# Kernel optimization log

Hardware: AMD Instinct MI355X
Metric: run time of the kernel (lower is better)

Reference implementation:

```python
import jax, jax.numpy as jnp
import numpy as np

NUM_HEADS = 8  # from init_kwargs

def _conv1x1(x, W, b):
    # x: [B, Cin, H, W], W: [Cout, Cin], b: [Cout]  (nn.Conv2d kernel_size=1)
    return jnp.einsum('bchw,oc->bohw', x, W) + b[None, :, None, None]

def setup_inputs() -> dict:
    key = jax.random.key(0)
    ks = jax.random.split(key, 9)
    B, C, H, W = 8, 256, 32, 32
    Ck, Cv, Co = 256, 256, 256
    s = 1.0 / np.sqrt(C)
    return {
        'x':  jax.random.normal(ks[0], (B, C, H, W), dtype=jnp.float32),
        'Wq': jax.random.normal(ks[1], (Ck, C), dtype=jnp.float32) * s,
        'bq': jax.random.normal(ks[2], (Ck,), dtype=jnp.float32) * 0.02,
        'Wk': jax.random.normal(ks[3], (Ck, C), dtype=jnp.float32) * s,
        'bk': jax.random.normal(ks[4], (Ck,), dtype=jnp.float32) * 0.02,
        'Wv': jax.random.normal(ks[5], (Cv, C), dtype=jnp.float32) * s,
        'bv': jax.random.normal(ks[6], (Cv,), dtype=jnp.float32) * 0.02,
        'Wo': jax.random.normal(ks[7], (Co, Cv), dtype=jnp.float32) * s,
        'bo': jax.random.normal(ks[8], (Co,), dtype=jnp.float32) * 0.02,
    }

def reference(x, Wq, bq, Wk, bk, Wv, bv, Wo, bo):
    B, C, H, W = x.shape
    q = _conv1x1(x, Wq, bq)  # [B, Ck, H, W]
    k = _conv1x1(x, Wk, bk)  # [B, Ck, H, W]
    v = _conv1x1(x, Wv, bv)  # [B, Cv, H, W]
    nh = NUM_HEADS
    dk = q.shape[1] // nh
    dv = v.shape[1] // nh
    N = H * W
    # split heads, flatten spatial dims into sequence
    q = q.reshape(B, nh, dk, N) * (dk ** -0.5)
    k = k.reshape(B, nh, dk, N)
    v = v.reshape(B, nh, dv, N)
    logits = jnp.einsum('bhdn,bhdm->bhnm', q, k)        # [B, nh, N, N]
    attn = jax.nn.softmax(logits, axis=-1)
    o = jnp.einsum('bhnm,bhdm->bhdn', attn, v)           # [B, nh, dv, N]
    o = o.reshape(B, nh * dv, H, W)
    return _conv1x1(o, Wo, bo)                           # [B, Co, H, W]
```

## Files before the change

### kernel.cpp

```cpp
#include <hip/hip_runtime.h>
#include <math.h>

typedef unsigned short u16;
typedef __attribute__((ext_vector_type(8))) unsigned short u16x8;
typedef __attribute__((ext_vector_type(8))) short s16x8;
typedef __attribute__((ext_vector_type(4))) float f32x4;

#define QK_SCALE (0.17677669529663687f * 1.4426950408889634f)

__device__ __forceinline__ unsigned cvt2(float lo, float hi) {
  unsigned r;
  asm("v_cvt_pk_bf16_f32 %0, %1, %2" : "=v"(r) : "v"(lo), "v"(hi));
  return r;
}
__device__ __forceinline__ u16 f2bf(float f) { return (u16)cvt2(f, f); }
__device__ __forceinline__ u16x8 ld16(const void* p) { u16x8 v; __builtin_memcpy(&v, p, 16); return v; }
__device__ __forceinline__ void st16(void* p, u16x8 v) { __builtin_memcpy(p, &v, 16); }
__device__ __forceinline__ void st16s(void* p, s16x8 v) { __builtin_memcpy(p, &v, 16); }
__device__ __forceinline__ void st4(void* p, unsigned v) { __builtin_memcpy(p, &v, 4); }
__device__ __forceinline__ f32x4 ldf4(const void* p) { f32x4 v; __builtin_memcpy(&v, p, 16); return v; }
__device__ __forceinline__ void stf4(void* p, f32x4 v) { __builtin_memcpy(p, &v, 16); }
__device__ __forceinline__ s16x8 frag16(const void* p) { s16x8 v; __builtin_memcpy(&v, p, 16); return v; }
__device__ __forceinline__ s16x8 pack8(f32x4 lo, f32x4 hi) {
  union { unsigned u[4]; s16x8 s; } c;
  c.u[0] = cvt2(lo.x, lo.y); c.u[1] = cvt2(lo.z, lo.w);
  c.u[2] = cvt2(hi.x, hi.y); c.u[3] = cvt2(hi.z, hi.w);
  return c.s;
}

__global__ __launch_bounds__(256) void r18_qkv(
    const float* __restrict__ x,
    const float* __restrict__ Wq, const float* __restrict__ bq,
    const float* __restrict__ Wk, const float* __restrict__ bk,
    const float* __restrict__ Wv, const float* __restrict__ bv,
    u16* __restrict__ qo, u16* __restrict__ ko, u16* __restrict__ vo)
{
  __shared__ u16 xt[64][264];
  __shared__ u16 wlds[192][40];

  const int t = threadIdx.x;
  const int ntile = blockIdx.x, hp = blockIdx.y, b = blockIdx.z;
  const int n0 = ntile * 64, h0 = hp * 2;
  const int w = t >> 6, lane = t & 63, l15 = lane & 15, quad = lane >> 4;

  {
    const float* xrow = x + ((size_t)b * 256 + t) * 1024 + n0;
#pragma unroll
    for (int i = 0; i < 64; i += 4) {
      const f32x4 a = ldf4(xrow + i);
      xt[i + 0][t] = f2bf(a.x); xt[i + 1][t] = f2bf(a.y);
      xt[i + 2][t] = f2bf(a.z); xt[i + 3][t] = f2bf(a.w);
    }
  }

  f32x4 acc[12];
#pragma unroll
  for (int i = 0; i < 12; ++i) acc[i] = (f32x4){0.f, 0.f, 0.f, 0.f};

  for (int ks = 0; ks < 8; ++ks) {
    __syncthreads();
    if (t < 192) {
      const int m = t >> 6, hh = (t >> 5) & 1, r = t & 31;
      const float* M = (m == 0) ? Wq : (m == 1) ? Wk : Wv;
      const float* src = M + (size_t)((h0 + hh) * 32 + r) * 256 + ks * 32;
      st16s(&wlds[t][0],  pack8(ldf4(src),      ldf4(src + 4)));
      st16s(&wlds[t][8],  pack8(ldf4(src + 8),  ldf4(src + 12)));
      st16s(&wlds[t][16], pack8(ldf4(src + 16), ldf4(src + 20)));
      st16s(&wlds[t][24], pack8(ldf4(src + 24), ldf4(src + 28)));
    }
    __syncthreads();

    const s16x8 bfrag = frag16(&xt[w * 16 + l15][ks * 32 + quad * 8]);
#pragma unroll
    for (int mt = 0; mt < 12; ++mt) {
      const s16x8 af = frag16(&wlds[mt * 16 + l15][quad * 8]);
      acc[mt] = __builtin_amdgcn_mfma_f32_16x16x32_bf16(af, bfrag, acc[mt], 0, 0, 0);
    }
  }

  const int n = n0 + w * 16 + l15;
  const int sig = n & 127;
  const int nperm = (n & ~127) | ((sig & 15) << 3) | (sig >> 4);
#pragma unroll
  for (int hh = 0; hh < 2; ++hh) {
    const int h = h0 + hh;
    const size_t bh = (size_t)(b * 8 + h);
    u16* qrow = qo + (bh * 1024 + n) * 32;
    u16* krow = ko + (bh * 1024 + n) * 32;
#pragma unroll
    for (int half = 0; half < 2; ++half) {
      const int d0 = half * 16 + quad * 4;
      const f32x4 aq = acc[hh * 2 + half];
      const f32x4 ak = acc[4 + hh * 2 + half];
      const f32x4 av = acc[8 + hh * 2 + half];
      st4(qrow + d0,     cvt2((aq.x + bq[h * 32 + d0 + 0]) * QK_SCALE,
                              (aq.y + bq[h * 32 + d0 + 1]) * QK_SCALE));
      st4(qrow + d0 + 2, cvt2((aq.z + bq[h * 32 + d0 + 2]) * QK_SCALE,
                              (aq.w + bq[h * 32 + d0 + 3]) * QK_SCALE));
      st4(krow + d0,     cvt2(ak.x + bk[h * 32 + d0 + 0],
                              ak.y + bk[h * 32 + d0 + 1]));
      st4(krow + d0 + 2, cvt2(ak.z + bk[h * 32 + d0 + 2],
                              ak.w + bk[h * 32 + d0 + 3]));
#pragma unroll
      for (int rr = 0; rr < 4; ++rr) {
        const int d = d0 + rr;
        vo[(bh * 32 + d) * 1024 + nperm] = f2bf(av[rr] + bv[h * 32 + d]);
      }
    }
  }
}

__global__ __launch_bounds__(256) void r18_attn(
    const u16* __restrict__ qw, const u16* __restrict__ kw,
    const u16* __restrict__ vw, float* __restrict__ out)
{
  __shared__ __align__(16) char smem[36352];
  u16 (*klds)[40]  = (u16(*)[40])smem;
  u16 (*vlds)[136] = (u16(*)[136])(smem + 10240);
  u16 (*plds)[136] = (u16(*)[136])(smem + 18944);
  float (*otf)[72] = (float(*)[72])smem;

  const int t = threadIdx.x;
  const int qtile = blockIdx.x;
  const int bh = blockIdx.y;
  const int w = t >> 6, lane = t & 63, l15 = lane & 15, quad = lane >> 4;

  const s16x8 qfrag = frag16(
      qw + ((size_t)bh * 1024 + qtile * 64 + w * 16 + l15) * 32 + quad * 8);

  f32x4 o0 = {0.f, 0.f, 0.f, 0.f}, o1 = {0.f, 0.f, 0.f, 0.f};
  float mrun[4], lrun[4];
#pragma unroll
  for (int r = 0; r < 4; ++r) { mrun[r] = -1e30f; lrun[r] = 0.f; }

  for (int kb = 0; kb < 8; ++kb) {
    {
      const u16* ks_ = kw + ((size_t)bh * 1024 + kb * 128 + (t >> 1)) * 32 + (t & 1) * 16;
      st16(&klds[t >> 1][(t & 1) * 16], ld16(ks_));
      st16(&klds[t >> 1][(t & 1) * 16 + 8], ld16(ks_ + 8));
      const u16* vs_ = vw + ((size_t)bh * 32 + (t >> 3)) * 1024 + kb * 128 + (t & 7) * 16;
      st16(&vlds[t >> 3][(t & 7) * 16], ld16(vs_));
      st16(&vlds[t >> 3][(t & 7) * 16 + 8], ld16(vs_ + 8));
    }
    __syncthreads();

    f32x4 s[8];
    const f32x4 zz = {0.f, 0.f, 0.f, 0.f};
#pragma unroll
    for (int nt2 = 0; nt2 < 8; ++nt2) {
      const s16x8 kf = frag16(&klds[nt2 * 16 + l15][quad * 8]);
      s[nt2] = __builtin_amdgcn_mfma_f32_16x16x32_bf16(qfrag, kf, zz, 0, 0, 0);
    }

#pragma unroll
    for (int r = 0; r < 4; ++r) {
      float mx = fmaxf(fmaxf(fmaxf(s[0][r], s[1][r]), fmaxf(s[2][r], s[3][r])),
                       fmaxf(fmaxf(s[4][r], s[5][r]), fmaxf(s[6][r], s[7][r])));
      mx = fmaxf(mx, __shfl_xor(mx, 1));
      mx = fmaxf(mx, __shfl_xor(mx, 2));
      mx = fmaxf(mx, __shfl_xor(mx, 4));
      mx = fmaxf(mx, __shfl_xor(mx, 8));
      const float mnew = fmaxf(mrun[r], mx);
      const float alpha = exp2f(mrun[r] - mnew);
      f32x4 plo, phi;
#pragma unroll
      for (int j = 0; j < 4; ++j) {
        plo[j] = exp2f(s[j][r] - mnew);
        phi[j] = exp2f(s[4 + j][r] - mnew);
      }
      float rs = ((plo.x + plo.y) + (plo.z + plo.w)) +
                 ((phi.x + phi.y) + (phi.z + phi.w));
      rs += __shfl_xor(rs, 1);
      rs += __shfl_xor(rs, 2);
      rs += __shfl_xor(rs, 4);
      rs += __shfl_xor(rs, 8);
      lrun[r] = lrun[r] * alpha + rs;
      mrun[r] = mnew;
      o0[r] *= alpha;
      o1[r] *= alpha;
      st16s(&plds[w * 16 + quad * 4 + r][l15 * 8], pack8(plo, phi));
    }

#pragma unroll
    for (int ks = 0; ks < 4; ++ks) {
      const s16x8 pf  = frag16(&plds[w * 16 + l15][ks * 32 + quad * 8]);
      const s16x8 vf0 = frag16(&vlds[l15][ks * 32 + quad * 8]);
      const s16x8 vf1 = frag16(&vlds[16 + l15][ks * 32 + quad * 8]);
      o0 = __builtin_amdgcn_mfma_f32_16x16x32_bf16(pf, vf0, o0, 0, 0, 0);
      o1 = __builtin_amdgcn_mfma_f32_16x16x32_bf16(pf, vf1, o1, 0, 0, 0);
    }
    __syncthreads();
  }

#pragma unroll
  for (int r = 0; r < 4; ++r) {
    const float inv = 1.0f / lrun[r];
    otf[l15][w * 16 + quad * 4 + r]      = o0[r] * inv;
    otf[16 + l15][w * 16 + quad * 4 + r] = o1[r] * inv;
  }
  __syncthreads();
  {
    const int dd = t >> 3, i = t & 7;
    const int b = bh >> 3, hh = bh & 7;
    float* dst = out + ((size_t)b * 256 + hh * 32 + dd) * 1024 + qtile * 64 + i * 8;
    f32x4 v0, v1;
#pragma unroll
    for (int jj = 0; jj < 4; ++jj) { v0[jj] = otf[dd][i * 8 + jj];
                                     v1[jj] = otf[dd][i * 8 + 4 + jj]; }
    stf4(dst, v0); stf4(dst + 4, v1);
  }
}

__global__ __launch_bounds__(256) void r18_oproj(
    const float* __restrict__ Wo, const float* __restrict__ bo,
    float* __restrict__ out)
{
  __shared__ u16 o2t[32][264];
  const int t = threadIdx.x;
  const int nt = blockIdx.x, b = blockIdx.y;
  const int w = t >> 6, lane = t & 63, l15 = lane & 15, quad = lane >> 4;

  {
    const float* src = out + ((size_t)b * 256 + t) * 1024 + nt * 32;
#pragma unroll
    for (int i = 0; i < 32; i += 4) {
      const f32x4 a = ldf4(src + i);
      o2t[i + 0][t] = f2bf(a.x); o2t[i + 1][t] = f2bf(a.y);
      o2t[i + 2][t] = f2bf(a.z); o2t[i + 3][t] = f2bf(a.w);
    }
  }
  __syncthreads();

  f32x4 acc[4][2];
#pragma unroll
  for (int mt = 0; mt < 4; ++mt) {
    acc[mt][0] = (f32x4){0.f, 0.f, 0.f, 0.f};
    acc[mt][1] = (f32x4){0.f, 0.f, 0.f, 0.f};
  }

  for (int ks = 0; ks < 8; ++ks) {
    const s16x8 b0 = frag16(&o2t[l15][ks * 32 + quad * 8]);
    const s16x8 b1 = frag16(&o2t[16 + l15][ks * 32 + quad * 8]);
#pragma unroll
    for (int mt = 0; mt < 4; ++mt) {
      const float* wsrc = Wo + (size_t)(w * 64 + mt * 16 + l15) * 256 + ks * 32 + quad * 8;
      const s16x8 af = pack8(ldf4(wsrc), ldf4(wsrc + 4));
      acc[mt][0] = __builtin_amdgcn_mfma_f32_16x16x32_bf16(af, b0, acc[mt][0], 0, 0, 0);
      acc[mt][1] = __builtin_amdgcn_mfma_f32_16x16x32_bf16(af, b1, acc[mt][1], 0, 0, 0);
    }
  }

#pragma unroll
  for (int mt = 0; mt < 4; ++mt) {
#pragma unroll
    for (int r = 0; r < 4; ++r) {
      const int oc = w * 64 + mt * 16 + quad * 4 + r;
      const float bov = bo[oc];
      out[((size_t)b * 256 + oc) * 1024 + nt * 32 + l15]      = acc[mt][0][r] + bov;
      out[((size_t)b * 256 + oc) * 1024 + nt * 32 + 16 + l15] = acc[mt][1][r] + bov;
    }
  }
}

extern "C" void kernel_launch(void* const* d_in, const int* in_sizes, int n_in,
                              void* d_out, int out_size, void* d_ws, size_t ws_size,
                              hipStream_t stream) {
  (void)in_sizes; (void)n_in; (void)out_size; (void)ws_size;
  const float* x  = (const float*)d_in[0];
  const float* Wq = (const float*)d_in[1];
  const float* bq = (const float*)d_in[2];
  const float* Wk = (const float*)d_in[3];
  const float* bk = (const float*)d_in[4];
  const float* Wv = (const float*)d_in[5];
  const float* bv = (const float*)d_in[6];
  const float* Wo = (const float*)d_in[7];
  const float* bo = (const float*)d_in[8];
  float* out = (float*)d_out;

  char* ws = (char*)d_ws;
  u16* qw = (u16*)(ws);
  u16* kw = (u16*)(ws + (4u << 20));
  u16* vw = (u16*)(ws + (8u << 20));

  r18_qkv<<<dim3(16, 4, 8), 256, 0, stream>>>(
      x, Wq, bq, Wk, bk, Wv, bv, qw, kw, vw);
  r18_attn<<<dim3(16, 64), 256, 0, stream>>>(qw, kw, vw, out);
  r18_oproj<<<dim3(32, 8), 256, 0, stream>>>(Wo, bo, out);
}
```

Measured before the change: 151.0 us.

## Transpose attention MFMAs to keep P in registers and prefetch K/V

The QK^T MFMA now computes the transposed score tile (K as A operand), so each lane holds one query column. That makes the softmax max and sum reductions cross-quad shuffles with a single running max per lane. Probabilities are packed straight from registers into the PV MFMA B operand, which removes the P round trip through LDS. V's key order in the QKV kernel is re-permuted to match this register layout. K/V tiles for the next block are register-prefetched while the current one computes, one barrier per iteration is dropped, and the output is written directly with strided stores instead of an LDS transpose. The risk is less coalesced output stores.

New measurement: 137.5 us. -8.9%, faster.

```diff
diff --git a/kernel.cpp b/kernel.cpp
--- a/kernel.cpp
+++ b/kernel.cpp
@@ -28,7 +28,7 @@
   return c.s;
 }
 
-__global__ __launch_bounds__(256) void r18_qkv(
+__global__ __launch_bounds__(256) void r19_qkv(
     const float* __restrict__ x,
     const float* __restrict__ Wq, const float* __restrict__ bq,
     const float* __restrict__ Wk, const float* __restrict__ bk,
@@ -80,7 +80,8 @@
 
   const int n = n0 + w * 16 + l15;
   const int sig = n & 127;
-  const int nperm = (n & ~127) | ((sig & 15) << 3) | (sig >> 4);
+  const int ntn = sig >> 4, q4 = (sig >> 2) & 3, rn = sig & 3;
+  const int nperm = (n & ~127) | ((ntn >> 1) << 5) | (q4 << 3) | ((ntn & 1) << 2) | rn;
 #pragma unroll
   for (int hh = 0; hh < 2; ++hh) {
     const int h = h0 + hh;
@@ -110,15 +111,12 @@
   }
 }
 
-__global__ __launch_bounds__(256) void r18_attn(
+__global__ __launch_bounds__(256) void r19_attn(
     const u16* __restrict__ qw, const u16* __restrict__ kw,
     const u16* __restrict__ vw, float* __restrict__ out)
 {
-  __shared__ __align__(16) char smem[36352];
-  u16 (*klds)[40]  = (u16(*)[40])smem;
-  u16 (*vlds)[136] = (u16(*)[136])(smem + 10240);
-  u16 (*plds)[136] = (u16(*)[136])(smem + 18944);
-  float (*otf)[72] = (float(*)[72])smem;
+  __shared__ u16 klds[128][40];
+  __shared__ u16 vlds[32][136];
 
   const int t = threadIdx.x;
   const int qtile = blockIdx.x;
@@ -128,19 +126,26 @@
   const s16x8 qfrag = frag16(
       qw + ((size_t)bh * 1024 + qtile * 64 + w * 16 + l15) * 32 + quad * 8);
 
+  const u16* kbase = kw + ((size_t)bh * 1024 + (t >> 1)) * 32 + (t & 1) * 16;
+  const u16* vbase = vw + ((size_t)bh * 32 + (t >> 3)) * 1024 + (t & 7) * 16;
+
+  u16x8 gk0 = ld16(kbase), gk1 = ld16(kbase + 8);
+  u16x8 gv0 = ld16(vbase), gv1 = ld16(vbase + 8);
+
   f32x4 o0 = {0.f, 0.f, 0.f, 0.f}, o1 = {0.f, 0.f, 0.f, 0.f};
-  float mrun[4], lrun[4];
-#pragma unroll
-  for (int r = 0; r < 4; ++r) { mrun[r] = -1e30f; lrun[r] = 0.f; }
+  float mrun = -1e30f, lrun = 0.f;
 
   for (int kb = 0; kb < 8; ++kb) {
-    {
-      const u16* ks_ = kw + ((size_t)bh * 1024 + kb * 128 + (t >> 1)) * 32 + (t & 1) * 16;
-      st16(&klds[t >> 1][(t & 1) * 16], ld16(ks_));
-      st16(&klds[t >> 1][(t & 1) * 16 + 8], ld16(ks_ + 8));
-      const u16* vs_ = vw + ((size_t)bh * 32 + (t >> 3)) * 1024 + kb * 128 + (t & 7) * 16;
-      st16(&vlds[t >> 3][(t & 7) * 16], ld16(vs_));
-      st16(&vlds[t >> 3][(t & 7) * 16 + 8], ld16(vs_ + 8));
+    if (kb) __syncthreads();
+    st16(&klds[t >> 1][(t & 1) * 16], gk0);
+    st16(&klds[t >> 1][(t & 1) * 16 + 8], gk1);
+    st16(&vlds[t >> 3][(t & 7) * 16], gv0);
+    st16(&vlds[t >> 3][(t & 7) * 16 + 8], gv1);
+    if (kb < 7) {
+      const u16* kn = kbase + (size_t)(kb + 1) * (128 * 32);
+      const u16* vn = vbase + (size_t)(kb + 1) * 128;
+      gk0 = ld16(kn); gk1 = ld16(kn + 8);
+      gv0 = ld16(vn); gv1 = ld16(vn + 8);
     }
     __syncthreads();
 
@@ -149,69 +154,56 @@
 #pragma unroll
     for (int nt2 = 0; nt2 < 8; ++nt2) {
       const s16x8 kf = frag16(&klds[nt2 * 16 + l15][quad * 8]);
-      s[nt2] = __builtin_amdgcn_mfma_f32_16x16x32_bf16(qfrag, kf, zz, 0, 0, 0);
-    }
-
-#pragma unroll
-    for (int r = 0; r < 4; ++r) {
-      float mx = fmaxf(fmaxf(fmaxf(s[0][r], s[1][r]), fmaxf(s[2][r], s[3][r])),
-                       fmaxf(fmaxf(s[4][r], s[5][r]), fmaxf(s[6][r], s[7][r])));
-      mx = fmaxf(mx, __shfl_xor(mx, 1));
-      mx = fmaxf(mx, __shfl_xor(mx, 2));
-      mx = fmaxf(mx, __shfl_xor(mx, 4));
-      mx = fmaxf(mx, __shfl_xor(mx, 8));
-      const float mnew = fmaxf(mrun[r], mx);
-      const float alpha = exp2f(mrun[r] - mnew);
-      f32x4 plo, phi;
-#pragma unroll
-      for (int j = 0; j < 4; ++j) {
-        plo[j] = exp2f(s[j][r] - mnew);
-        phi[j] = exp2f(s[4 + j][r] - mnew);
+      s[nt2] = __builtin_amdgcn_mfma_f32_16x16x32_bf16(kf, qfrag, zz, 0, 0, 0);
+    }
+
+    float mx = fmaxf(fmaxf(s[0][0], s[0][1]), fmaxf(s[0][2], s[0][3]));
+#pragma unroll
+    for (int nt2 = 1; nt2 < 8; ++nt2)
+      mx = fmaxf(mx, fmaxf(fmaxf(s[nt2][0], s[nt2][1]),
+                           fmaxf(s[nt2][2], s[nt2][3])));
+    mx = fmaxf(mx, __shfl_xor(mx, 16));
+    mx = fmaxf(mx, __shfl_xor(mx, 32));
+    const float mnew = fmaxf(mrun, mx);
+    const float alpha = exp2f(mrun - mnew);
+    float rs = 0.f;
+#pragma unroll
+    for (int nt2 = 0; nt2 < 8; ++nt2) {
+#pragma unroll
+      for (int r = 0; r < 4; ++r) {
+        s[nt2][r] = exp2f(s[nt2][r] - mnew);
+        rs += s[nt2][r];
       }
-      float rs = ((plo.x + plo.y) + (plo.z + plo.w)) +
-                 ((phi.x + phi.y) + (phi.z + phi.w));
-      rs += __shfl_xor(rs, 1);
-      rs += __shfl_xor(rs, 2);
-      rs += __shfl_xor(rs, 4);
-      rs += __shfl_xor(rs, 8);
-      lrun[r] = lrun[r] * alpha + rs;
-      mrun[r] = mnew;
-      o0[r] *= alpha;
-      o1[r] *= alpha;
-      st16s(&plds[w * 16 + quad * 4 + r][l15 * 8], pack8(plo, phi));
-    }
+    }
+    rs += __shfl_xor(rs, 16);
+    rs += __shfl_xor(rs, 32);
+    lrun = lrun * alpha + rs;
+    mrun = mnew;
+#pragma unroll
+    for (int r = 0; r < 4; ++r) { o0[r] *= alpha; o1[r] *= alpha; }
 
 #pragma unroll
     for (int ks = 0; ks < 4; ++ks) {
-      const s16x8 pf  = frag16(&plds[w * 16 + l15][ks * 32 + quad * 8]);
+      const s16x8 pf  = pack8(s[2 * ks], s[2 * ks + 1]);
       const s16x8 vf0 = frag16(&vlds[l15][ks * 32 + quad * 8]);
       const s16x8 vf1 = frag16(&vlds[16 + l15][ks * 32 + quad * 8]);
-      o0 = __builtin_amdgcn_mfma_f32_16x16x32_bf16(pf, vf0, o0, 0, 0, 0);
-      o1 = __builtin_amdgcn_mfma_f32_16x16x32_bf16(pf, vf1, o1, 0, 0, 0);
-    }
-    __syncthreads();
-  }
-
+      o0 = __builtin_amdgcn_mfma_f32_16x16x32_bf16(vf0, pf, o0, 0, 0, 0);
+      o1 = __builtin_amdgcn_mfma_f32_16x16x32_bf16(vf1, pf, o1, 0, 0, 0);
+    }
+  }
+
+  const float inv = 1.0f / lrun;
+  const int b = bh >> 3, hh = bh & 7;
+  float* obase = out + ((size_t)b * 256 + hh * 32) * 1024
+               + qtile * 64 + w * 16 + l15;
 #pragma unroll
   for (int r = 0; r < 4; ++r) {
-    const float inv = 1.0f / lrun[r];
-    otf[l15][w * 16 + quad * 4 + r]      = o0[r] * inv;
-    otf[16 + l15][w * 16 + quad * 4 + r] = o1[r] * inv;
-  }
-  __syncthreads();
-  {
-    const int dd = t >> 3, i = t & 7;
-    const int b = bh >> 3, hh = bh & 7;
-    float* dst = out + ((size_t)b * 256 + hh * 32 + dd) * 1024 + qtile * 64 + i * 8;
-    f32x4 v0, v1;
-#pragma unroll
-    for (int jj = 0; jj < 4; ++jj) { v0[jj] = otf[dd][i * 8 + jj];
-                                     v1[jj] = otf[dd][i * 8 + 4 + jj]; }
-    stf4(dst, v0); stf4(dst + 4, v1);
-  }
-}
-
-__global__ __launch_bounds__(256) void r18_oproj(
+    obase[(size_t)(quad * 4 + r) * 1024]      = o0[r] * inv;
+    obase[(size_t)(16 + quad * 4 + r) * 1024] = o1[r] * inv;
+  }
+}
+
+__global__ __launch_bounds__(256) void r19_oproj(
     const float* __restrict__ Wo, const float* __restrict__ bo,
     float* __restrict__ out)
 {
@@ -282,8 +274,8 @@
   u16* kw = (u16*)(ws + (4u << 20));
   u16* vw = (u16*)(ws + (8u << 20));
 
-  r18_qkv<<<dim3(16, 4, 8), 256, 0, stream>>>(
+  r19_qkv<<<dim3(16, 4, 8), 256, 0, stream>>>(
       x, Wq, bq, Wk, bk, Wv, bv, qw, kw, vw);
-  r18_attn<<<dim3(16, 64), 256, 0, stream>>>(qw, kw, vw, out);
-  r18_oproj<<<dim3(32, 8), 256, 0, stream>>>(Wo, bo, out);
-}
+  r19_attn<<<dim3(16, 64), 256, 0, stream>>>(qw, kw, vw, out);
+  r19_oproj<<<dim3(32, 8), 256, 0, stream>>>(Wo, bo, out);
+}
```
